# Performance work log

Hardware: AMD Instinct MI355X
Metric: run time of the kernel (lower is better)

## Reference

```python
import jax, jax.numpy as jnp
import numpy as np

N_NODES = 100000
N_EDGES = 1600000
IN_C, HID_C, OUT_C = 64, 64, 32


def setup_inputs() -> dict:
    key = jax.random.key(0)
    ks = jax.random.split(key, 10)
    return {
        "x": jax.random.normal(ks[0], (N_NODES, IN_C), dtype=jnp.float32),
        "edge_index": jax.random.randint(ks[1], (2, N_EDGES), 0, N_NODES, dtype=jnp.int32),
        "W_l": jax.random.normal(ks[2], (IN_C, HID_C), dtype=jnp.float32) * 0.1,
        "W_r": jax.random.normal(ks[3], (IN_C, HID_C), dtype=jnp.float32) * 0.1,
        "b1": jax.random.normal(ks[4], (HID_C,), dtype=jnp.float32) * 0.1,
        "W_g": jax.random.normal(ks[5], (HID_C, OUT_C), dtype=jnp.float32) * 0.1,
        "att_src": jax.random.normal(ks[6], (OUT_C,), dtype=jnp.float32) * 0.1,
        "att_dst": jax.random.normal(ks[7], (OUT_C,), dtype=jnp.float32) * 0.1,
        "b2": jax.random.normal(ks[8], (OUT_C,), dtype=jnp.float32) * 0.1,
    }


def _gnn(x, edge_index, W_l, W_r, b1, W_g, att_src, att_dst, b2):
    n = x.shape[0]
    src, dst = edge_index[0], edge_index[1]

    # --- SAGEConv: mean neighbor aggregation + root transform ---
    deg = jax.ops.segment_sum(jnp.ones_like(src, dtype=x.dtype), dst, num_segments=n)
    agg = jax.ops.segment_sum(x[src], dst, num_segments=n)  # [N, IN_C]
    agg = agg / jnp.maximum(deg, 1.0)[:, None]
    h = agg @ W_l + b1 + x @ W_r
    h = jax.nn.relu(h)
    # dropout(p=0.5) is identity in eval mode

    # --- GATConv (heads=1), with self-loops (PyG default) ---
    loop = jnp.arange(n, dtype=src.dtype)
    s = jnp.concatenate([src, loop])
    d = jnp.concatenate([dst, loop])
    z = h @ W_g                      # [N, OUT_C]
    a_s = z @ att_src                # [N] per-node source score
    a_d = z @ att_dst                # [N] per-node dest score
    e = jax.nn.leaky_relu(a_s[s] + a_d[d], negative_slope=0.2)  # [E+N]
    # segment softmax over edges grouped by destination node
    m = jax.ops.segment_max(e, d, num_segments=n)
    ex = jnp.exp(e - m[d])
    denom = jax.ops.segment_sum(ex, d, num_segments=n)
    alpha = ex / denom[d]
    out = jax.ops.segment_sum(alpha[:, None] * z[s], d, num_segments=n) + b2

    return jax.nn.log_softmax(out, axis=1)


def reference(x, edge_index, W_l, W_r, b1, W_g, att_src, att_dst, b2):
    return _gnn(x, edge_index, W_l, W_r, b1, W_g, att_src, att_dst, b2)
```

## Files before the change

### kernel.cpp

```cpp
#include <hip/hip_runtime.h>
#include <cstdint>
#include <cstddef>


typedef unsigned short ushort_t;
typedef unsigned int uint_t;
typedef __attribute__((ext_vector_type(8))) short short8;
typedef __attribute__((ext_vector_type(4))) float f32x4;
typedef __attribute__((ext_vector_type(2))) float f32x2;

__device__ inline ushort_t f2bf(float f) {
    uint_t u = __float_as_uint(f);
    uint_t r = (u + 0x7fffu + ((u >> 16) & 1u)) >> 16;
    return (ushort_t)r;
}
__device__ inline uint_t pkbf(float a, float b) {
    return (uint_t)f2bf(a) | ((uint_t)f2bf(b) << 16);
}

#define PART_CHUNK 8192


__global__ __launch_bounds__(256) void k_pre(const float* __restrict__ x, ushort_t* __restrict__ xh,
                                             unsigned char* __restrict__ xq,
                                             const int* __restrict__ ei, int* __restrict__ tot,
                                             int* __restrict__ cnt,
                                             const float* __restrict__ Wl, const float* __restrict__ Wr,
                                             const float* __restrict__ Wg,
                                             ushort_t* __restrict__ Wlrt, ushort_t* __restrict__ Wgt,
                                             unsigned char* __restrict__ zq,
                                             int n4, int E, int NB, int N, int nchunk) {
    __shared__ int h[512];
    int bid = blockIdx.x, tid = threadIdx.x;
    int idx = bid * 256 + tid;
    if (idx < n4) {
        float4 v = ((const float4*)x)[idx];
        ushort4 o = { f2bf(v.x), f2bf(v.y), f2bf(v.z), f2bf(v.w) };
        ((ushort4*)xh)[idx] = o;
        int r = 0;
        r = __builtin_amdgcn_cvt_pk_fp8_f32(v.x, v.y, r, false);
        r = __builtin_amdgcn_cvt_pk_fp8_f32(v.z, v.w, r, true);
        ((uint_t*)xq)[idx] = (uint_t)r;
    }
    if (bid < nchunk) {
        for (int b = tid; b < NB; b += 256) h[b] = 0;
        __syncthreads();
        int b0 = bid * PART_CHUNK;
        int b1 = min(b0 + PART_CHUNK, E);
        for (int j = b0 + tid; j < b1; j += 256) atomicAdd(&h[ei[E + j] >> 8], 1);
        __syncthreads();
        int* crow = cnt + (size_t)bid * NB;
        for (int b = tid; b < NB; b += 256) {
            int hb = h[b];
            crow[b] = hb;
            if (hb) atomicAdd(&tot[b], hb);
        }
    } else if (bid == nchunk) {
        if (tid < 16) ((uint_t*)(xq + (size_t)N * 64))[tid] = 0;
        if (tid < 8)  ((uint_t*)(zq + (size_t)N * 32))[tid] = 0;
    } else if (bid >= 512 && bid < 544) {
        int t = (bid - 512) * 256 + tid;
        int n = t >> 7, k = t & 127;
        float v = (k < 64) ? Wl[k * 64 + n] : Wr[(k - 64) * 64 + n];
        Wlrt[n * 128 + k] = f2bf(v);
        if (t < 32 * 64) {
            int n2 = t >> 6, k2 = t & 63;
            Wgt[n2 * 64 + k2] = f2bf(Wg[k2 * 32 + n2]);
        }
    }
}


__global__ __launch_bounds__(256) void k_scan(const int* __restrict__ tot, int* __restrict__ base,
                                              int* __restrict__ gofs, int* __restrict__ rowptr,
                                              int NB, int E, int N) {
    __shared__ int t[256];
    int tid = threadIdx.x;
    int v0 = (2 * tid < NB) ? tot[2 * tid] : 0;
    int v1 = (2 * tid + 1 < NB) ? tot[2 * tid + 1] : 0;
    t[tid] = v0 + v1;
    __syncthreads();
    for (int off = 1; off < 256; off <<= 1) {
        int u = (tid >= off) ? t[tid - off] : 0;
        __syncthreads();
        t[tid] += u;
        __syncthreads();
    }
    int pairExcl = (tid > 0) ? t[tid - 1] : 0;
    if (2 * tid < NB)     { base[2 * tid] = pairExcl;          gofs[2 * tid] = pairExcl; }
    if (2 * tid + 1 < NB) { base[2 * tid + 1] = pairExcl + v0; gofs[2 * tid + 1] = pairExcl + v0; }
    if (tid == 0) { rowptr[N] = E; base[NB] = E; }
}


__global__ __launch_bounds__(256) void k_part(const int* __restrict__ ei, const int* __restrict__ cnt,
                                              int* __restrict__ gofs,
                                              uint_t* __restrict__ pairs, int E, int NB) {
    __shared__ int ofs[512];
    int tid = threadIdx.x;
    const int* crow = cnt + (size_t)blockIdx.x * NB;
    for (int b = tid; b < NB; b += 256) {
        int hb = crow[b];
        ofs[b] = hb ? atomicAdd(&gofs[b], hb) : 0;
    }
    __syncthreads();
    int b0 = blockIdx.x * PART_CHUNK;
    int b1 = min(b0 + PART_CHUNK, E);
    for (int j = b0 + tid; j < b1; j += 256) {
        int d = ei[E + j], s = ei[j];
        int p = atomicAdd(&ofs[d >> 8], 1);
        pairs[p] = (uint_t)s | ((uint_t)(d & 255) << 24);
    }
}


__global__ __launch_bounds__(256) void k_csr(const uint_t* __restrict__ pairs, const int* __restrict__ base,
                                             int* __restrict__ rowptr, int* __restrict__ csr, int N) {
    __shared__ int h[256];
    __shared__ int s[256];
    int b = blockIdx.x;
    int d0 = b << 8;
    int e0 = base[b], e1 = base[b + 1];
    int tid = threadIdx.x;
    h[tid] = 0;
    __syncthreads();
    for (int j = e0 + tid; j < e1; j += 256) atomicAdd(&h[pairs[j] >> 24], 1);
    __syncthreads();
    int v = h[tid];
    s[tid] = v;
    __syncthreads();
    for (int off = 1; off < 256; off <<= 1) {
        int u = (tid >= off) ? s[tid - off] : 0;
        __syncthreads();
        s[tid] += u;
        __syncthreads();
    }
    int excl = s[tid] - v;
    if (d0 + tid < N) rowptr[d0 + tid] = e0 + excl;
    __syncthreads();
    h[tid] = e0 + excl;
    __syncthreads();
    for (int j = e0 + tid; j < e1; j += 256) {
        uint_t p = pairs[j];
        int pos = atomicAdd(&h[p >> 24], 1);
        csr[pos] = (int)(p & 0xffffffu);
    }
}


__global__ __launch_bounds__(256) void k_gather(const int* __restrict__ rowptr, const int* __restrict__ csr,
                                                const unsigned char* __restrict__ xq,
                                                ushort_t* __restrict__ aggh, int N) {
    __shared__ int scr[256];
    int tid = threadIdx.x;
    int l = tid & 15, g = tid >> 4;
    int i = blockIdx.x * 16 + g;
    if (i >= N) return;
    int r0 = rowptr[i], r1 = rowptr[i + 1];
    int sub = l >> 3, lc = l & 7;
    const char* xb = (const char*)xq + lc * 8;
    float a0 = 0.f, a1 = 0.f, a2 = 0.f, a3 = 0.f;
    float a4 = 0.f, a5 = 0.f, a6 = 0.f, a7 = 0.f;
    for (int bb = r0; bb < r1; bb += 16) {
        int idx = bb + l;
        int src = (idx < r1) ? csr[idx] : N;
        scr[tid] = src << 6;
        uint4 q0 = *(const uint4*)&scr[g * 16 + 0];
        uint4 q1 = *(const uint4*)&scr[g * 16 + 4];
        uint4 q2 = *(const uint4*)&scr[g * 16 + 8];
        uint4 q3 = *(const uint4*)&scr[g * 16 + 12];
#define HSTEP(oa, ob) { \
        uint_t off = sub ? (ob) : (oa); \
        uint2 u = *(const uint2*)(xb + off); \
        f32x2 p0 = __builtin_amdgcn_cvt_pk_f32_fp8((int)u.x, false); \
        f32x2 p1 = __builtin_amdgcn_cvt_pk_f32_fp8((int)u.x, true); \
        f32x2 p2 = __builtin_amdgcn_cvt_pk_f32_fp8((int)u.y, false); \
        f32x2 p3 = __builtin_amdgcn_cvt_pk_f32_fp8((int)u.y, true); \
        a0 += p0.x; a1 += p0.y; a2 += p1.x; a3 += p1.y; \
        a4 += p2.x; a5 += p2.y; a6 += p3.x; a7 += p3.y; }
        HSTEP(q0.x, q0.y) HSTEP(q0.z, q0.w)
        HSTEP(q1.x, q1.y) HSTEP(q1.z, q1.w)
        HSTEP(q2.x, q2.y) HSTEP(q2.z, q2.w)
        HSTEP(q3.x, q3.y) HSTEP(q3.z, q3.w)
#undef HSTEP
    }
    a0 += __shfl_xor(a0, 8, 64); a1 += __shfl_xor(a1, 8, 64);
    a2 += __shfl_xor(a2, 8, 64); a3 += __shfl_xor(a3, 8, 64);
    a4 += __shfl_xor(a4, 8, 64); a5 += __shfl_xor(a5, 8, 64);
    a6 += __shfl_xor(a6, 8, 64); a7 += __shfl_xor(a7, 8, 64);
    if (sub == 0) {
        float dn = 1.0f / fmaxf((float)(r1 - r0), 1.0f);
        uint4 o = { pkbf(a0 * dn, a1 * dn), pkbf(a2 * dn, a3 * dn),
                    pkbf(a4 * dn, a5 * dn), pkbf(a6 * dn, a7 * dn) };
        *(uint4*)(aggh + (size_t)i * 64 + lc * 8) = o;
    }
}


__global__ __launch_bounds__(256) void k_gemm(const ushort_t* __restrict__ aggh, const ushort_t* __restrict__ xh,
                                              const ushort_t* __restrict__ Wlrt, const ushort_t* __restrict__ Wgt,
                                              const float* __restrict__ b1,
                                              const float* __restrict__ att_src, const float* __restrict__ att_dst,
                                              unsigned char* __restrict__ zq, float* __restrict__ a_s,
                                              float* __restrict__ a_d, int N) {
    __shared__ ushort_t Wls[64 * 136];
    __shared__ ushort_t Wgs[32 * 72];
    __shared__ ushort_t hs[64 * 136];
    int tid = threadIdx.x;
    for (int t = tid; t < 64 * 16; t += 256) {
        int n = t >> 4, cq = t & 15;
        *(uint4*)(&Wls[n * 136 + cq * 8]) = *(const uint4*)(&Wlrt[n * 128 + cq * 8]);
    }
    for (int t = tid; t < 32 * 8; t += 256) {
        int n = t >> 3, cq = t & 7;
        *(uint4*)(&Wgs[n * 72 + cq * 8]) = *(const uint4*)(&Wgt[n * 64 + cq * 8]);
    }
    __syncthreads();

    int w = tid >> 6, lane = tid & 63;
    int c = lane & 15, quad = lane >> 4;
    int m0 = blockIdx.x * 64 + w * 16;
    int row = m0 + c;
    bool rowok = row < N;

    f32x4 acc[4] = {};
    #pragma unroll
    for (int kk = 0; kk < 4; ++kk) {
        const ushort_t* Abase = (kk < 2) ? aggh : xh;
        int koff = (kk & 1) * 32 + quad * 8;
        short8 a = {};
        if (rowok) a = *(const short8*)(Abase + (size_t)row * 64 + koff);
        #pragma unroll
        for (int nb = 0; nb < 4; ++nb) {
            short8 b = *(const short8*)(&Wls[(nb * 16 + c) * 136 + kk * 32 + quad * 8]);
            acc[nb] = __builtin_amdgcn_mfma_f32_16x16x32_bf16(a, b, acc[nb], 0, 0, 0);
        }
    }
    ushort_t* hw = &hs[w * 16 * 136];
    #pragma unroll
    for (int nb = 0; nb < 4; ++nb) {
        float bb = b1[nb * 16 + c];
        #pragma unroll
        for (int r = 0; r < 4; ++r) {
            float h = acc[nb][r] + bb;
            hw[(quad * 4 + r) * 136 + nb * 16 + c] = f2bf(fmaxf(h, 0.f));
        }
    }
    f32x4 acc2[2] = {};
    #pragma unroll
    for (int kk = 0; kk < 2; ++kk) {
        short8 a = *(const short8*)(&hw[c * 136 + kk * 32 + quad * 8]);
        #pragma unroll
        for (int nb = 0; nb < 2; ++nb) {
            short8 b = *(const short8*)(&Wgs[(nb * 16 + c) * 72 + kk * 32 + quad * 8]);
            acc2[nb] = __builtin_amdgcn_mfma_f32_16x16x32_bf16(a, b, acc2[nb], 0, 0, 0);
        }
    }
    float as0 = att_src[c], as1 = att_src[16 + c];
    float ad0 = att_dst[c], ad1 = att_dst[16 + c];
    #pragma unroll
    for (int r = 0; r < 4; ++r) {
        int grow = m0 + quad * 4 + r;
        float z0 = acc2[0][r], z1 = acc2[1][r];
        float ps = z0 * as0 + z1 * as1;
        float pd = z0 * ad0 + z1 * ad1;
        #pragma unroll
        for (int off = 8; off; off >>= 1) {
            ps += __shfl_xor(ps, off, 64);
            pd += __shfl_xor(pd, off, 64);
        }
        if (grow < N) {
            int r8 = __builtin_amdgcn_cvt_pk_fp8_f32(z0, z1, 0, false);
            unsigned char* zrow = zq + (size_t)grow * 32;
            zrow[c] = (unsigned char)(r8 & 0xff);
            zrow[16 + c] = (unsigned char)((r8 >> 8) & 0xff);
            if (c == 0) { a_s[grow] = ps; a_d[grow] = pd; }
        }
    }
}


__global__ __launch_bounds__(256) void k_gat(const unsigned char* __restrict__ zq, const float* __restrict__ a_s,
                                             const float* __restrict__ a_d, const int* __restrict__ rowptr,
                                             const int* __restrict__ csr, const float* __restrict__ b2,
                                             float* __restrict__ out, int N) {
    __shared__ uint2 scr[256];
    int tid = threadIdx.x;
    int l = tid & 15, g = tid >> 4;
    int i = blockIdx.x * 16 + g;
    if (i >= N) return;
    int r0 = rowptr[i], r1 = rowptr[i + 1];
    float adi = a_d[i], asi = a_s[i];
    int sub = l >> 3, lc = l & 7;
    const char* zb = (const char*)zq + lc * 4;
    float a0 = 0.f, a1 = 0.f, a2 = 0.f, a3 = 0.f, dsum = 0.f;

    for (int bb = r0; bb < r1; bb += 16) {
        int idx = bb + l;
        bool valid = idx < r1;
        int s_l = valid ? csr[idx] : N;
        float w_l = 0.f;
        if (valid) {
            float e = a_s[s_l] + adi;
            e = fmaxf(e, 0.2f * e);
            w_l = __expf(e);
            dsum += w_l;
        }
        scr[tid] = make_uint2((uint_t)(s_l << 5), __float_as_uint(w_l));
        #pragma unroll
        for (int r = 0; r < 8; ++r) {
            uint4 q = *(const uint4*)&scr[g * 16 + r * 2];
            uint_t off = sub ? q.z : q.x;
            float w = __uint_as_float(sub ? q.w : q.y);
            uint_t u = *(const uint_t*)(zb + off);
            f32x2 p0 = __builtin_amdgcn_cvt_pk_f32_fp8((int)u, false);
            f32x2 p1 = __builtin_amdgcn_cvt_pk_f32_fp8((int)u, true);
            a0 += w * p0.x; a1 += w * p0.y;
            a2 += w * p1.x; a3 += w * p1.y;
        }
    }
    #pragma unroll
    for (int off = 8; off; off >>= 1) dsum += __shfl_xor(dsum, off, 64);
    a0 += __shfl_xor(a0, 8, 64); a1 += __shfl_xor(a1, 8, 64);
    a2 += __shfl_xor(a2, 8, 64); a3 += __shfl_xor(a3, 8, 64);
    float es = asi + adi; es = fmaxf(es, 0.2f * es);
    float wse = __expf(es);
    float denom = dsum + wse;
    uint_t us = *(const uint_t*)((const char*)zq + (size_t)i * 32 + lc * 4);
    f32x2 s0 = __builtin_amdgcn_cvt_pk_f32_fp8((int)us, false);
    f32x2 s1 = __builtin_amdgcn_cvt_pk_f32_fp8((int)us, true);
    a0 += wse * s0.x; a1 += wse * s0.y;
    a2 += wse * s1.x; a3 += wse * s1.y;

    float rden = 1.0f / denom;
    float o0 = a0 * rden + b2[lc * 4 + 0];
    float o1 = a1 * rden + b2[lc * 4 + 1];
    float o2 = a2 * rden + b2[lc * 4 + 2];
    float o3 = a3 * rden + b2[lc * 4 + 3];
    float m2 = fmaxf(fmaxf(o0, o1), fmaxf(o2, o3));
    #pragma unroll
    for (int off = 4; off; off >>= 1) m2 = fmaxf(m2, __shfl_xor(m2, off, 64));
    float ssum = __expf(o0 - m2) + __expf(o1 - m2) + __expf(o2 - m2) + __expf(o3 - m2);
    #pragma unroll
    for (int off = 4; off; off >>= 1) ssum += __shfl_xor(ssum, off, 64);
    float lg = m2 + __logf(ssum);
    if (sub == 0) {
        float4 r = { o0 - lg, o1 - lg, o2 - lg, o3 - lg };
        *(float4*)(out + (size_t)i * 32 + lc * 4) = r;
    }
}


extern "C" void kernel_launch(void* const* d_in, const int* in_sizes, int n_in,
                              void* d_out, int out_size, void* d_ws, size_t ws_size,
                              hipStream_t stream) {
    const float* x       = (const float*)d_in[0];
    const int*   ei      = (const int*)d_in[1];
    const float* Wl      = (const float*)d_in[2];
    const float* Wr      = (const float*)d_in[3];
    const float* b1      = (const float*)d_in[4];
    const float* Wg      = (const float*)d_in[5];
    const float* att_src = (const float*)d_in[6];
    const float* att_dst = (const float*)d_in[7];
    const float* b2      = (const float*)d_in[8];
    float* out = (float*)d_out;

    int N = in_sizes[0] / 64;
    int E = in_sizes[1] / 2;
    int NB = (N + 255) >> 8;
    int nchunk = (E + PART_CHUNK - 1) / PART_CHUNK;

    char* ws = (char*)d_ws;
    size_t off = 0;
    auto alloc = [&](size_t bytes) { size_t r = off; off += (bytes + 255) & ~(size_t)255; return r; };
    int* tot       = (int*)(ws + alloc((size_t)(NB + 1) * 4));
    int* base      = (int*)(ws + alloc((size_t)(NB + 1) * 4));
    int* gofs      = (int*)(ws + alloc((size_t)(NB + 1) * 4));
    int* cnt       = (int*)(ws + alloc((size_t)nchunk * NB * 4));
    int* rowptr    = (int*)(ws + alloc((size_t)(N + 1) * 4));
    uint_t* pairs  = (uint_t*)(ws + alloc((size_t)E * 4));
    int* csr       = (int*)(ws + alloc((size_t)E * 4));
    ushort_t* xh   = (ushort_t*)(ws + alloc((size_t)N * 64 * 2));
    unsigned char* xq = (unsigned char*)(ws + alloc((size_t)(N + 1) * 64));
    ushort_t* aggh = (ushort_t*)(ws + alloc((size_t)N * 64 * 2));
    unsigned char* zq = (unsigned char*)(ws + alloc((size_t)(N + 1) * 32));
    float* a_s     = (float*)(ws + alloc((size_t)N * 4));
    float* a_d     = (float*)(ws + alloc((size_t)N * 4));
    ushort_t* Wlrt = (ushort_t*)(ws + alloc(64 * 128 * 2));
    ushort_t* Wgt  = (ushort_t*)(ws + alloc(32 * 64 * 2));

    (void)hipMemsetAsync(tot, 0, (size_t)NB * 4, stream);

    int n4 = N * 64 / 4;
    int gpre = (n4 + 255) / 256;
    if (gpre < 545) gpre = 545;
    k_pre    <<<gpre, 256, 0, stream>>>(x, xh, xq, ei, tot, cnt, Wl, Wr, Wg, Wlrt, Wgt, zq, n4, E, NB, N, nchunk);
    k_scan   <<<1, 256, 0, stream>>>(tot, base, gofs, rowptr, NB, E, N);
    k_part   <<<nchunk, 256, 0, stream>>>(ei, cnt, gofs, pairs, E, NB);
    k_csr    <<<NB, 256, 0, stream>>>(pairs, base, rowptr, csr, N);
    k_gather <<<(N + 15) / 16, 256, 0, stream>>>(rowptr, csr, xq, aggh, N);
    k_gemm   <<<(N + 63) / 64, 256, 0, stream>>>(aggh, xh, Wlrt, Wgt, b1, att_src, att_dst, zq, a_s, a_d, N);
    k_gat    <<<(N + 15) / 16, 256, 0, stream>>>(zq, a_s, a_d, rowptr, csr, b2, out, N);
}
```

Measured before the change: 198.9 us.

## Fold bucket scan into partition kernel and drop global atomics and memset

```diff
diff --git a/kernel.cpp b/kernel.cpp
--- a/kernel.cpp
+++ b/kernel.cpp
@@ -23,7 +23,7 @@
 
 __global__ __launch_bounds__(256) void k_pre(const float* __restrict__ x, ushort_t* __restrict__ xh,
                                              unsigned char* __restrict__ xq,
-                                             const int* __restrict__ ei, int* __restrict__ tot,
+                                             const int* __restrict__ ei,
                                              int* __restrict__ cnt,
                                              const float* __restrict__ Wl, const float* __restrict__ Wr,
                                              const float* __restrict__ Wg,
@@ -50,11 +50,7 @@
         for (int j = b0 + tid; j < b1; j += 256) atomicAdd(&h[ei[E + j] >> 8], 1);
         __syncthreads();
         int* crow = cnt + (size_t)bid * NB;
-        for (int b = tid; b < NB; b += 256) {
-            int hb = h[b];
-            crow[b] = hb;
-            if (hb) atomicAdd(&tot[b], hb);
-        }
+        for (int b = tid; b < NB; b += 256) crow[b] = h[b];
     } else if (bid == nchunk) {
         if (tid < 16) ((uint_t*)(xq + (size_t)N * 64))[tid] = 0;
         if (tid < 8)  ((uint_t*)(zq + (size_t)N * 32))[tid] = 0;
@@ -71,13 +67,27 @@
 }
 
 
-__global__ __launch_bounds__(256) void k_scan(const int* __restrict__ tot, int* __restrict__ base,
-                                              int* __restrict__ gofs, int* __restrict__ rowptr,
-                                              int NB, int E, int N) {
+__global__ __launch_bounds__(256) void k_part(const int* __restrict__ ei, const int* __restrict__ cnt,
+                                              int* __restrict__ base, int* __restrict__ rowptr,
+                                              uint_t* __restrict__ pairs, int E, int NB, int N,
+                                              int nchunk) {
+    __shared__ int tot_s[512];
+    __shared__ int ofs[512];
     __shared__ int t[256];
-    int tid = threadIdx.x;
-    int v0 = (2 * tid < NB) ? tot[2 * tid] : 0;
-    int v1 = (2 * tid + 1 < NB) ? tot[2 * tid + 1] : 0;
+    int tid = threadIdx.x, bid = blockIdx.x;
+    for (int b = tid; b < NB; b += 256) {
+        int tsum = 0, moff = 0;
+        for (int c = 0; c < nchunk; ++c) {
+            int v = cnt[(size_t)c * NB + b];
+            tsum += v;
+            if (c < bid) moff += v;
+        }
+        tot_s[b] = tsum;
+        ofs[b] = moff;
+    }
+    __syncthreads();
+    int v0 = (2 * tid < NB) ? tot_s[2 * tid] : 0;
+    int v1 = (2 * tid + 1 < NB) ? tot_s[2 * tid + 1] : 0;
     t[tid] = v0 + v1;
     __syncthreads();
     for (int off = 1; off < 256; off <<= 1) {
@@ -87,24 +97,17 @@
         __syncthreads();
     }
     int pairExcl = (tid > 0) ? t[tid - 1] : 0;
-    if (2 * tid < NB)     { base[2 * tid] = pairExcl;          gofs[2 * tid] = pairExcl; }
-    if (2 * tid + 1 < NB) { base[2 * tid + 1] = pairExcl + v0; gofs[2 * tid + 1] = pairExcl + v0; }
-    if (tid == 0) { rowptr[N] = E; base[NB] = E; }
-}
-
-
-__global__ __launch_bounds__(256) void k_part(const int* __restrict__ ei, const int* __restrict__ cnt,
-                                              int* __restrict__ gofs,
-                                              uint_t* __restrict__ pairs, int E, int NB) {
-    __shared__ int ofs[512];
-    int tid = threadIdx.x;
-    const int* crow = cnt + (size_t)blockIdx.x * NB;
-    for (int b = tid; b < NB; b += 256) {
-        int hb = crow[b];
-        ofs[b] = hb ? atomicAdd(&gofs[b], hb) : 0;
-    }
-    __syncthreads();
-    int b0 = blockIdx.x * PART_CHUNK;
+    if (2 * tid < NB) {
+        ofs[2 * tid] += pairExcl;
+        if (bid == 0) base[2 * tid] = pairExcl;
+    }
+    if (2 * tid + 1 < NB) {
+        ofs[2 * tid + 1] += pairExcl + v0;
+        if (bid == 0) base[2 * tid + 1] = pairExcl + v0;
+    }
+    if (bid == 0 && tid == 0) { base[NB] = E; rowptr[N] = E; }
+    __syncthreads();
+    int b0 = bid * PART_CHUNK;
     int b1 = min(b0 + PART_CHUNK, E);
     for (int j = b0 + tid; j < b1; j += 256) {
         int d = ei[E + j], s = ei[j];
@@ -373,9 +376,7 @@
     char* ws = (char*)d_ws;
     size_t off = 0;
     auto alloc = [&](size_t bytes) { size_t r = off; off += (bytes + 255) & ~(size_t)255; return r; };
-    int* tot       = (int*)(ws + alloc((size_t)(NB + 1) * 4));
     int* base      = (int*)(ws + alloc((size_t)(NB + 1) * 4));
-    int* gofs      = (int*)(ws + alloc((size_t)(NB + 1) * 4));
     int* cnt       = (int*)(ws + alloc((size_t)nchunk * NB * 4));
     int* rowptr    = (int*)(ws + alloc((size_t)(N + 1) * 4));
     uint_t* pairs  = (uint_t*)(ws + alloc((size_t)E * 4));
@@ -389,14 +390,11 @@
     ushort_t* Wlrt = (ushort_t*)(ws + alloc(64 * 128 * 2));
     ushort_t* Wgt  = (ushort_t*)(ws + alloc(32 * 64 * 2));
 
-    (void)hipMemsetAsync(tot, 0, (size_t)NB * 4, stream);
-
     int n4 = N * 64 / 4;
     int gpre = (n4 + 255) / 256;
     if (gpre < 545) gpre = 545;
-    k_pre    <<<gpre, 256, 0, stream>>>(x, xh, xq, ei, tot, cnt, Wl, Wr, Wg, Wlrt, Wgt, zq, n4, E, NB, N, nchunk);
-    k_scan   <<<1, 256, 0, stream>>>(tot, base, gofs, rowptr, NB, E, N);
-    k_part   <<<nchunk, 256, 0, stream>>>(ei, cnt, gofs, pairs, E, NB);
+    k_pre    <<<gpre, 256, 0, stream>>>(x, xh, xq, ei, cnt, Wl, Wr, Wg, Wlrt, Wgt, zq, n4, E, NB, N, nchunk);
+    k_part   <<<nchunk, 256, 0, stream>>>(ei, cnt, base, rowptr, pairs, E, NB, N, nchunk);
     k_csr    <<<NB, 256, 0, stream>>>(pairs, base, rowptr, csr, N);
     k_gather <<<(N + 15) / 16, 256, 0, stream>>>(rowptr, csr, xq, aggh, N);
     k_gemm   <<<(N + 63) / 64, 256, 0, stream>>>(aggh, xh, Wlrt, Wgt, b1, att_src, att_dst, zq, a_s, a_d, N);
```

New measurement: 275.2 us. +38.4%, slower.
